# Optimization experiments

Hardware: AMD Instinct MI355X
Metric: run time of the kernel (lower is better)

## Reference

```python
import jax, jax.numpy as jnp
import numpy as np

SIG = 10
C = 0.0
STD = 1.0
N_ATOMS = 21
N_TRAIN = 8192
DESC = N_ATOMS * (N_ATOMS - 1) // 2  # 210
M = 64


def setup_inputs() -> dict:
    key = jax.random.key(0)
    k1, k2, k3 = jax.random.split(key, 3)
    Rs = jax.random.normal(k1, (M, N_ATOMS, 3), dtype=jnp.float32)
    xs_train = jax.random.uniform(k2, (N_TRAIN, DESC), dtype=jnp.float32)
    Jx_alphas = jax.random.normal(k3, (N_TRAIN, DESC), dtype=jnp.float32)
    return {"Rs": Rs, "xs_train": xs_train, "Jx_alphas": Jx_alphas}


def reference(Rs, xs_train, Jx_alphas):
    sig = SIG
    q = np.sqrt(5.0) / sig
    n = N_ATOMS
    # pairwise atom displacements / distances: [M, n, n, 3], [M, n, n]
    diffs = Rs[:, :, None, :] - Rs[:, None, :, :]
    dists = jnp.linalg.norm(diffs, axis=-1)
    eye = jnp.eye(n, dtype=bool)
    dists = jnp.where(eye, jnp.inf, dists)  # kill diagonal
    i, j = np.tril_indices(n, k=-1)
    xs = 1.0 / dists[:, i, j]                       # [M, D] inverse-distance descriptor
    x_diffs = q * xs[:, None, :] - q * xs_train     # [M, T, D]
    x_dists = jnp.linalg.norm(x_diffs, axis=-1)     # [M, T]
    exp_xs = (5.0 / (3.0 * sig ** 2)) * jnp.exp(-x_dists)
    dot = jnp.einsum('mtd,td->mt', x_diffs, Jx_alphas)
    exp_xs_1 = exp_xs * (1.0 + x_dists)
    F1s_x = jnp.einsum('mt,mtd->md', exp_xs * dot, x_diffs)  # [M, D]
    F2s_x = exp_xs_1 @ Jx_alphas                              # [M, D]
    Fs_x = (F1s_x - F2s_x) * STD
    # expand_tril: scatter D lower-tri values to symmetric [M, n, n], zero diag
    full = jnp.zeros((Fs_x.shape[0], n, n), dtype=Fs_x.dtype)
    full = full.at[:, i, j].set(Fs_x).at[:, j, i].set(Fs_x)
    Fs = jnp.einsum('mab,mabc->mac', full / dists ** 3, diffs)  # diag: 0/inf -> 0
    Es = jnp.sum(exp_xs_1 * dot, axis=-1) / q
    Es = C + Es * STD
    return Es, Fs
```

## Files before the change

kernel.cpp:

```cpp
#include <hip/hip_runtime.h>
#include <math.h>

#define NA   21
#define NM   64
#define ND   210
#define DP   224
#define NT   8192
#define NCH  28
#define KS2  32

#define QC 0.22360679774997896f
#define KE 0.016666666666666666f

typedef short bf8 __attribute__((ext_vector_type(8)));
typedef float f4  __attribute__((ext_vector_type(4)));

#define O_XF   0u
#define O_JF   917504u
#define O_XFT  1835008u
#define O_JFT  2752512u
#define O_W1   3670016u
#define O_E1   3932160u
#define O_AF   4194304u
#define O_QG   4201472u
#define O_NTT  4215808u
#define O_CJ   4224000u
#define O_NX   4232192u
#define O_PB   4261056u
#define O_ESP  5178560u
#define O_WAP  5211328u

__device__ __forceinline__ unsigned short f2bf(float f) {
    unsigned u = __float_as_uint(f);
    u += 0x7fffu + ((u >> 16) & 1u);
    return (unsigned short)(u >> 16);
}
__device__ __forceinline__ float bf2f(unsigned short h) {
    return __uint_as_float((unsigned)h << 16);
}

__device__ __forceinline__ void d_to_ij(int d, int& i, int& j) {
    int ii = (int)((1.0f + sqrtf(1.0f + 8.0f * (float)d)) * 0.5f);
    while (ii * (ii - 1) / 2 > d) --ii;
    while ((ii + 1) * ii / 2 <= d) ++ii;
    i = ii;
    j = d - ii * (ii - 1) / 2;
}

__global__ __launch_bounds__(256) void k_prep(
    const float* __restrict__ Rs, const float* __restrict__ xs,
    const float* __restrict__ Jx,
    unsigned short* __restrict__ Xf, unsigned short* __restrict__ Jf,
    unsigned short* __restrict__ XfT, unsigned short* __restrict__ JfT,
    unsigned short* __restrict__ Af, float* __restrict__ qxsG,
    float* __restrict__ nx, float* __restrict__ nt, float* __restrict__ cJ) {
    const int b = blockIdx.x, tid = threadIdx.x;
    __shared__ float lds[2 * 16 * 210];

    if (b < 512) {
        const int t0 = b * 16;
        const float4* sx = (const float4*)(xs + (size_t)t0 * ND);
        const float4* sj = (const float4*)(Jx + (size_t)t0 * ND);
#pragma unroll
        for (int k = 0; k < 4; ++k) {
            const int i = k * 256 + tid;
            if (i < 840) {
                ((float4*)lds)[i] = sx[i];
                ((float4*)(lds + 3360))[i] = sj[i];
            }
        }
        __syncthreads();
#pragma unroll
        for (int k = 0; k < 7; ++k) {
            const int idx = k * 256 + tid;
            if (idx < 896) {
                const int arr = idx / 448;
                const int rem = idx - arr * 448;
                const int kq = rem >> 4, colt = rem & 15;
                const float* src = lds + arr * 3360 + colt * 210;
                const float sc = arr ? 1.0f : QC;
                union { unsigned short us[8]; uint4 v; } u;
#pragma unroll
                for (int i = 0; i < 8; ++i) {
                    const int d = kq * 8 + i;
                    u.us[i] = (d < ND) ? f2bf(sc * src[d]) : (unsigned short)0;
                }
                *(uint4*)((arr ? Jf : Xf) + ((size_t)(b * NCH + kq) * 16 + colt) * 8) = u.v;
            } else {
                const int idx2 = idx - 896;
                const int arr = idx2 / 448;
                const int rem = idx2 - arr * 448;
                const int dtile = rem >> 5;
                const int rem2 = rem & 31;
                const int tql = rem2 >> 4, col = rem2 & 15;
                const int d = dtile * 16 + col;
                const float* src = lds + arr * 3360 + tql * 8 * 210;
                const float sc = arr ? 1.0f : QC;
                union { unsigned short us[8]; uint4 v; } u;
#pragma unroll
                for (int i = 0; i < 8; ++i)
                    u.us[i] = (d < ND) ? f2bf(sc * src[i * 210 + d])
                                       : (unsigned short)0;
                const size_t off = ((size_t)(dtile * 1024 + b * 2 + tql) * 16 + col) * 8;
                *(uint4*)((arr ? JfT : XfT) + off) = u.v;
            }
        }
        const int tt = tid >> 4, l = tid & 15;
        const float* xr = lds + tt * 210;
        const float* jr = lds + 3360 + tt * 210;
        float sn = 0.0f, sc2 = 0.0f;
        for (int c = l; c < ND; c += 16) {
            float x = bf2f(f2bf(QC * xr[c]));
            float j = bf2f(f2bf(jr[c]));
            sn = fmaf(x, x, sn);
            sc2 = fmaf(x, j, sc2);
        }
#pragma unroll
        for (int off = 1; off < 16; off <<= 1) {
            sn += __shfl_xor(sn, off);
            sc2 += __shfl_xor(sc2, off);
        }
        if (l == 0) {
            nt[t0 + tt] = sn;
            cJ[t0 + tt] = sc2;
        }
    } else {
        const int m = b - 512;
        float* R = lds;
        float* red = lds + 64;
        if (tid < NA * 3) R[tid] = Rs[m * NA * 3 + tid];
        __syncthreads();
        float local = 0.0f;
        if (tid < DP) {
            float vr = 0.0f;
            unsigned short hv = 0;
            if (tid < ND) {
                int i, j; d_to_ij(tid, i, j);
                float dx = R[i * 3] - R[j * 3];
                float dy = R[i * 3 + 1] - R[j * 3 + 1];
                float dz = R[i * 3 + 2] - R[j * 3 + 2];
                float v = QC / sqrtf(dx * dx + dy * dy + dz * dz);
                hv = f2bf(v);
                vr = bf2f(hv);
            }
            Af[(((m >> 4) * NCH + (tid >> 3)) * 16 + (m & 15)) * 8 + (tid & 7)] = hv;
            qxsG[(tid >> 2) * 256 + m * 4 + (tid & 3)] = vr;
            local = vr * vr;
        }
        red[tid] = local;
        __syncthreads();
        for (int s = 128; s > 0; s >>= 1) {
            if (tid < s) red[tid] += red[tid + s];
            __syncthreads();
        }
        if (tid == 0) nx[m] = red[0];
    }
}

__global__ __launch_bounds__(256) void k_stage1(
    const unsigned short* __restrict__ Af, const unsigned short* __restrict__ Xf,
    const unsigned short* __restrict__ Jf, const float* __restrict__ nt,
    const float* __restrict__ cJ, const float* __restrict__ nx,
    unsigned short* __restrict__ w1f, unsigned short* __restrict__ e1f,
    float* __restrict__ EsPart, float* __restrict__ WaPart) {
    const int tid = threadIdx.x;
    const int lane = tid & 63;
    const int w = tid >> 6;
    const int col = lane & 15, quad = lane >> 4;
    const int ttile = blockIdx.x;
    __shared__ float Dw[64][17];
    __shared__ float De[64][17];

    const unsigned short* ap = Af + ((size_t)(w * NCH + quad) * 16 + col) * 8;
    const unsigned short* xp = Xf + ((size_t)(ttile * NCH + quad) * 16 + col) * 8;
    const unsigned short* jp = Jf + ((size_t)(ttile * NCH + quad) * 16 + col) * 8;

    bf8 af[7];
#pragma unroll
    for (int kc = 0; kc < 7; ++kc) af[kc] = *(const bf8*)(ap + kc * 512);

    bf8 bx[2], bj[2];
    bx[0] = *(const bf8*)xp;
    bj[0] = *(const bf8*)jp;
    bx[1] = *(const bf8*)(xp + 512);
    bj[1] = *(const bf8*)(jp + 512);

    f4 c1 = {0.f, 0.f, 0.f, 0.f};
    f4 c2 = {0.f, 0.f, 0.f, 0.f};
#pragma unroll
    for (int kc = 0; kc < 7; ++kc) {
        const int s = kc & 1;
        c1 = __builtin_amdgcn_mfma_f32_16x16x32_bf16(af[kc], bx[s], c1, 0, 0, 0);
        c2 = __builtin_amdgcn_mfma_f32_16x16x32_bf16(af[kc], bj[s], c2, 0, 0, 0);
        if (kc < 5) {
            bx[s] = *(const bf8*)(xp + (kc + 2) * 512);
            bj[s] = *(const bf8*)(jp + (kc + 2) * 512);
        }
    }

    const int t = ttile * 16 + col;
    const float ntv = nt[t], cjv = cJ[t];
    float esA[4], wlA[4];
#pragma unroll
    for (int r = 0; r < 4; ++r) {
        const int m = w * 16 + quad * 4 + r;
        float sq = fmaxf(nx[m] - 2.0f * c1[r] + ntv, 0.0f);
        float xd = sqrtf(sq);
        float e = KE * expf(-xd);
        float dotv = c2[r] - cjv;
        float wv = e * dotv;
        float ev = e * (1.0f + xd);
        Dw[m][col] = wv;
        De[m][col] = ev;
        esA[r] = ev * dotv;
        wlA[r] = wv;
    }
    __syncthreads();
    {
        const int aidx = tid >> 7;
        const int c = tid & 127;
        const int mtile = c >> 5, tql = (c >> 4) & 1, colm = c & 15;
        const float* srcD = aidx ? &De[0][0] : &Dw[0][0];
        unsigned short* dst = aidx ? e1f : w1f;
        const int m = mtile * 16 + colm;
        union { unsigned short us[8]; uint4 v; } u;
#pragma unroll
        for (int i = 0; i < 8; ++i) u.us[i] = f2bf(srcD[m * 17 + tql * 8 + i]);
        const size_t off = ((size_t)(mtile * 1024 + ttile * 2 + tql) * 16 + colm) * 8;
        *(uint4*)(dst + off) = u.v;
    }
#pragma unroll
    for (int r = 0; r < 4; ++r) {
        float e = esA[r], wl = wlA[r];
#pragma unroll
        for (int off = 1; off < 16; off <<= 1) {
            e += __shfl_xor(e, off);
            wl += __shfl_xor(wl, off);
        }
        if (col == 0) {
            const int m = w * 16 + quad * 4 + r;
            EsPart[(size_t)m * 512 + ttile] = e;
            WaPart[(size_t)m * 512 + ttile] = wl;
        }
    }
}

__global__ __launch_bounds__(256) void k_stage2(
    const unsigned short* __restrict__ w1f, const unsigned short* __restrict__ e1f,
    const unsigned short* __restrict__ XfT, const unsigned short* __restrict__ JfT,
    float* __restrict__ Pbuf) {
    const int tid = threadIdx.x;
    const int lane = tid & 63;
    const int w = tid >> 6;
    const int col = lane & 15, quad = lane >> 4;
    const int dt = blockIdx.x;
    const int by = blockIdx.y;

    const unsigned short* awp = w1f + ((size_t)(w * 1024 + by * 32 + quad) * 16 + col) * 8;
    const unsigned short* aep = e1f + ((size_t)(w * 1024 + by * 32 + quad) * 16 + col) * 8;
    const unsigned short* bxp = XfT + ((size_t)(dt * 1024 + by * 32 + quad) * 16 + col) * 8;
    const unsigned short* bjp = JfT + ((size_t)(dt * 1024 + by * 32 + quad) * 16 + col) * 8;

    bf8 aw[2], ae[2], bx[2], bj[2];
    aw[0] = *(const bf8*)awp;         ae[0] = *(const bf8*)aep;
    bx[0] = *(const bf8*)bxp;         bj[0] = *(const bf8*)bjp;
    aw[1] = *(const bf8*)(awp + 512); ae[1] = *(const bf8*)(aep + 512);
    bx[1] = *(const bf8*)(bxp + 512); bj[1] = *(const bf8*)(bjp + 512);

    f4 dA = {0.f, 0.f, 0.f, 0.f};
    f4 dB = {0.f, 0.f, 0.f, 0.f};
#pragma unroll
    for (int kk = 0; kk < 8; ++kk) {
        const int s = kk & 1;
        dA = __builtin_amdgcn_mfma_f32_16x16x32_bf16(aw[s], bx[s], dA, 0, 0, 0);
        dB = __builtin_amdgcn_mfma_f32_16x16x32_bf16(ae[s], bj[s], dB, 0, 0, 0);
        if (kk < 6) {
            aw[s] = *(const bf8*)(awp + (kk + 2) * 512);
            ae[s] = *(const bf8*)(aep + (kk + 2) * 512);
            bx[s] = *(const bf8*)(bxp + (kk + 2) * 512);
            bj[s] = *(const bf8*)(bjp + (kk + 2) * 512);
        }
    }
    float* p = Pbuf + (size_t)by * 28672 + dt * 16 + col;
#pragma unroll
    for (int r = 0; r < 4; ++r) {
        const int m = w * 16 + quad * 4 + r;
        p[m * DP] = dA[r];
        p[14336 + m * DP] = dB[r];
    }
}

__global__ void k_final(const float* __restrict__ Rs, const float* __restrict__ qxsG,
                        const float* __restrict__ Pbuf, const float* __restrict__ EsPart,
                        const float* __restrict__ WaPart, float* __restrict__ out) {
    int m = blockIdx.x, tid = threadIdx.x;
    __shared__ float R[NA * 3];
    __shared__ float Ff[NA][NA];
    __shared__ float redE[256];
    __shared__ float redW[256];
    __shared__ float ABs[DP];
    if (tid < NA * 3) R[tid] = Rs[m * NA * 3 + tid];
    if (tid < NA) Ff[tid][tid] = 0.0f;
    if (tid < DP) {
        const float* p0 = Pbuf + (size_t)m * DP + tid;
        float s1 = 0.0f, s2 = 0.0f;
#pragma unroll
        for (int ks = 0; ks < KS2; ++ks) {
            s1 += p0[(size_t)ks * 28672];
            s2 += p0[(size_t)ks * 28672 + 14336];
        }
        ABs[tid] = s1 + s2;
    }
    {
        const float2 ep = ((const float2*)(EsPart + (size_t)m * 512))[tid];
        const float2 wp = ((const float2*)(WaPart + (size_t)m * 512))[tid];
        redE[tid] = ep.x + ep.y;
        redW[tid] = wp.x + wp.y;
    }
    __syncthreads();
    for (int s = 128; s > 0; s >>= 1) {
        if (tid < s) {
            redE[tid] += redE[tid + s];
            redW[tid] += redW[tid + s];
        }
        __syncthreads();
    }
    const float Wa = redW[0];
    if (tid < ND) {
        int i, j; d_to_ij(tid, i, j);
        float dx = R[i * 3] - R[j * 3];
        float dy = R[i * 3 + 1] - R[j * 3 + 1];
        float dz = R[i * 3 + 2] - R[j * 3 + 2];
        float dist2 = dx * dx + dy * dy + dz * dz;
        float fsx = qxsG[(tid >> 2) * 256 + m * 4 + (tid & 3)] * Wa - ABs[tid];
        float f = fsx / (dist2 * sqrtf(dist2));
        Ff[i][j] = f;
        Ff[j][i] = f;
    }
    __syncthreads();
    if (tid < NA * 3) {
        int a = tid / 3, c = tid % 3;
        float s = 0.0f;
        for (int b = 0; b < NA; ++b) {
            if (b == a) continue;
            s += Ff[a][b] * (R[a * 3 + c] - R[b * 3 + c]);
        }
        out[NM + m * NA * 3 + tid] = s;
    }
    if (tid == 0) out[m] = redE[0] / QC;
}

extern "C" void kernel_launch(void* const* d_in, const int* in_sizes, int n_in,
                              void* d_out, int out_size, void* d_ws, size_t ws_size,
                              hipStream_t stream) {
    const float* Rs = (const float*)d_in[0];
    const float* xs_train = (const float*)d_in[1];
    const float* Jx_alphas = (const float*)d_in[2];
    float* out = (float*)d_out;
    float* ws = (float*)d_ws;

    unsigned short* Xf  = (unsigned short*)(ws + O_XF);
    unsigned short* Jf  = (unsigned short*)(ws + O_JF);
    unsigned short* XfT = (unsigned short*)(ws + O_XFT);
    unsigned short* JfT = (unsigned short*)(ws + O_JFT);
    unsigned short* w1f = (unsigned short*)(ws + O_W1);
    unsigned short* e1f = (unsigned short*)(ws + O_E1);
    unsigned short* Af  = (unsigned short*)(ws + O_AF);
    float* qxsG   = ws + O_QG;
    float* nt     = ws + O_NTT;
    float* cJ     = ws + O_CJ;
    float* nx     = ws + O_NX;
    float* Pbuf   = ws + O_PB;
    float* EsPart = ws + O_ESP;
    float* WaPart = ws + O_WAP;

    k_prep<<<576, 256, 0, stream>>>(Rs, xs_train, Jx_alphas, Xf, Jf, XfT, JfT,
                                    Af, qxsG, nx, nt, cJ);
    k_stage1<<<512, 256, 0, stream>>>(Af, Xf, Jf, nt, cJ, nx, w1f, e1f, EsPart, WaPart);
    k_stage2<<<dim3(14, KS2), 256, 0, stream>>>(w1f, e1f, XfT, JfT, Pbuf);
    k_final<<<NM, 256, 0, stream>>>(Rs, qxsG, Pbuf, EsPart, WaPart, out);
}
```

Baseline: 92.78 us.

## Fuse train-data bf16 conversion into stage1 via swizzled LDS tiles

Splits the geometry part of the prep kernel into its own small kernel and moves the xs/Jx conversion into the stage1 kernel. Each stage1 block now loads its 16 training rows, converts them to bf16 in an XOR-swizzled LDS buffer, computes the norms locally, and feeds the MFMA B operands from LDS. This drops the Xf/Jf/nt/cJ global round trip. The cost is more LDS per block and extra in-kernel conversion work ahead of the MFMA loop.

```diff
diff --git a/kernel.cpp b/kernel.cpp
--- a/kernel.cpp
+++ b/kernel.cpp
@@ -15,16 +15,12 @@
 typedef short bf8 __attribute__((ext_vector_type(8)));
 typedef float f4  __attribute__((ext_vector_type(4)));
 
-#define O_XF   0u
-#define O_JF   917504u
 #define O_XFT  1835008u
 #define O_JFT  2752512u
 #define O_W1   3670016u
 #define O_E1   3932160u
 #define O_AF   4194304u
 #define O_QG   4201472u
-#define O_NTT  4215808u
-#define O_CJ   4224000u
 #define O_NX   4232192u
 #define O_PB   4261056u
 #define O_ESP  5178560u
@@ -47,144 +43,139 @@
     j = d - ii * (ii - 1) / 2;
 }
 
-__global__ __launch_bounds__(256) void k_prep(
-    const float* __restrict__ Rs, const float* __restrict__ xs,
-    const float* __restrict__ Jx,
-    unsigned short* __restrict__ Xf, unsigned short* __restrict__ Jf,
+__global__ __launch_bounds__(256) void k_geom(
+    const float* __restrict__ Rs, unsigned short* __restrict__ Af,
+    float* __restrict__ qxsG, float* __restrict__ nx) {
+    const int m = blockIdx.x, tid = threadIdx.x;
+    __shared__ float R[NA * 3];
+    __shared__ float red[256];
+    if (tid < NA * 3) R[tid] = Rs[m * NA * 3 + tid];
+    __syncthreads();
+    float local = 0.0f;
+    if (tid < DP) {
+        float vr = 0.0f;
+        unsigned short hv = 0;
+        if (tid < ND) {
+            int i, j; d_to_ij(tid, i, j);
+            float dx = R[i * 3] - R[j * 3];
+            float dy = R[i * 3 + 1] - R[j * 3 + 1];
+            float dz = R[i * 3 + 2] - R[j * 3 + 2];
+            float v = QC / sqrtf(dx * dx + dy * dy + dz * dz);
+            hv = f2bf(v);
+            vr = bf2f(hv);
+        }
+        Af[(((m >> 4) * NCH + (tid >> 3)) * 16 + (m & 15)) * 8 + (tid & 7)] = hv;
+        qxsG[(tid >> 2) * 256 + m * 4 + (tid & 3)] = vr;
+        local = vr * vr;
+    }
+    red[tid] = local;
+    __syncthreads();
+    for (int s = 128; s > 0; s >>= 1) {
+        if (tid < s) red[tid] += red[tid + s];
+        __syncthreads();
+    }
+    if (tid == 0) nx[m] = red[0];
+}
+
+__global__ __launch_bounds__(256) void k_s1p(
+    const float* __restrict__ xs, const float* __restrict__ Jx,
+    const unsigned short* __restrict__ Af, const float* __restrict__ nxg,
     unsigned short* __restrict__ XfT, unsigned short* __restrict__ JfT,
-    unsigned short* __restrict__ Af, float* __restrict__ qxsG,
-    float* __restrict__ nx, float* __restrict__ nt, float* __restrict__ cJ) {
-    const int b = blockIdx.x, tid = threadIdx.x;
-    __shared__ float lds[2 * 16 * 210];
-
-    if (b < 512) {
-        const int t0 = b * 16;
-        const float4* sx = (const float4*)(xs + (size_t)t0 * ND);
-        const float4* sj = (const float4*)(Jx + (size_t)t0 * ND);
-#pragma unroll
-        for (int k = 0; k < 4; ++k) {
-            const int i = k * 256 + tid;
-            if (i < 840) {
-                ((float4*)lds)[i] = sx[i];
-                ((float4*)(lds + 3360))[i] = sj[i];
-            }
-        }
-        __syncthreads();
-#pragma unroll
-        for (int k = 0; k < 7; ++k) {
-            const int idx = k * 256 + tid;
-            if (idx < 896) {
-                const int arr = idx / 448;
-                const int rem = idx - arr * 448;
-                const int kq = rem >> 4, colt = rem & 15;
-                const float* src = lds + arr * 3360 + colt * 210;
-                const float sc = arr ? 1.0f : QC;
-                union { unsigned short us[8]; uint4 v; } u;
-#pragma unroll
-                for (int i = 0; i < 8; ++i) {
-                    const int d = kq * 8 + i;
-                    u.us[i] = (d < ND) ? f2bf(sc * src[d]) : (unsigned short)0;
-                }
-                *(uint4*)((arr ? Jf : Xf) + ((size_t)(b * NCH + kq) * 16 + colt) * 8) = u.v;
-            } else {
-                const int idx2 = idx - 896;
-                const int arr = idx2 / 448;
-                const int rem = idx2 - arr * 448;
-                const int dtile = rem >> 5;
-                const int rem2 = rem & 31;
-                const int tql = rem2 >> 4, col = rem2 & 15;
-                const int d = dtile * 16 + col;
-                const float* src = lds + arr * 3360 + tql * 8 * 210;
-                const float sc = arr ? 1.0f : QC;
-                union { unsigned short us[8]; uint4 v; } u;
-#pragma unroll
-                for (int i = 0; i < 8; ++i)
-                    u.us[i] = (d < ND) ? f2bf(sc * src[i * 210 + d])
-                                       : (unsigned short)0;
-                const size_t off = ((size_t)(dtile * 1024 + b * 2 + tql) * 16 + col) * 8;
-                *(uint4*)((arr ? JfT : XfT) + off) = u.v;
-            }
-        }
-        const int tt = tid >> 4, l = tid & 15;
-        const float* xr = lds + tt * 210;
-        const float* jr = lds + 3360 + tt * 210;
-        float sn = 0.0f, sc2 = 0.0f;
-        for (int c = l; c < ND; c += 16) {
-            float x = bf2f(f2bf(QC * xr[c]));
-            float j = bf2f(f2bf(jr[c]));
-            sn = fmaf(x, x, sn);
-            sc2 = fmaf(x, j, sc2);
-        }
-#pragma unroll
-        for (int off = 1; off < 16; off <<= 1) {
-            sn += __shfl_xor(sn, off);
-            sc2 += __shfl_xor(sc2, off);
-        }
-        if (l == 0) {
-            nt[t0 + tt] = sn;
-            cJ[t0 + tt] = sc2;
-        }
-    } else {
-        const int m = b - 512;
-        float* R = lds;
-        float* red = lds + 64;
-        if (tid < NA * 3) R[tid] = Rs[m * NA * 3 + tid];
-        __syncthreads();
-        float local = 0.0f;
-        if (tid < DP) {
-            float vr = 0.0f;
-            unsigned short hv = 0;
-            if (tid < ND) {
-                int i, j; d_to_ij(tid, i, j);
-                float dx = R[i * 3] - R[j * 3];
-                float dy = R[i * 3 + 1] - R[j * 3 + 1];
-                float dz = R[i * 3 + 2] - R[j * 3 + 2];
-                float v = QC / sqrtf(dx * dx + dy * dy + dz * dz);
-                hv = f2bf(v);
-                vr = bf2f(hv);
-            }
-            Af[(((m >> 4) * NCH + (tid >> 3)) * 16 + (m & 15)) * 8 + (tid & 7)] = hv;
-            qxsG[(tid >> 2) * 256 + m * 4 + (tid & 3)] = vr;
-            local = vr * vr;
-        }
-        red[tid] = local;
-        __syncthreads();
-        for (int s = 128; s > 0; s >>= 1) {
-            if (tid < s) red[tid] += red[tid + s];
-            __syncthreads();
-        }
-        if (tid == 0) nx[m] = red[0];
-    }
-}
-
-__global__ __launch_bounds__(256) void k_stage1(
-    const unsigned short* __restrict__ Af, const unsigned short* __restrict__ Xf,
-    const unsigned short* __restrict__ Jf, const float* __restrict__ nt,
-    const float* __restrict__ cJ, const float* __restrict__ nx,
     unsigned short* __restrict__ w1f, unsigned short* __restrict__ e1f,
     float* __restrict__ EsPart, float* __restrict__ WaPart) {
-    const int tid = threadIdx.x;
+    const int b = blockIdx.x, tid = threadIdx.x;
     const int lane = tid & 63;
     const int w = tid >> 6;
     const int col = lane & 15, quad = lane >> 4;
-    const int ttile = blockIdx.x;
+
+    __shared__ unsigned short xJh[2 * 16 * DP];
     __shared__ float Dw[64][17];
     __shared__ float De[64][17];
+    __shared__ float ntL[16], cjL[16];
+    char* xB = (char*)xJh;
 
     const unsigned short* ap = Af + ((size_t)(w * NCH + quad) * 16 + col) * 8;
-    const unsigned short* xp = Xf + ((size_t)(ttile * NCH + quad) * 16 + col) * 8;
-    const unsigned short* jp = Jf + ((size_t)(ttile * NCH + quad) * 16 + col) * 8;
-
     bf8 af[7];
 #pragma unroll
     for (int kc = 0; kc < 7; ++kc) af[kc] = *(const bf8*)(ap + kc * 512);
-
+    float nxv[4];
+#pragma unroll
+    for (int r = 0; r < 4; ++r) nxv[r] = nxg[w * 16 + quad * 4 + r];
+
+    if (tid < 224) {
+        const int arr = tid / 112, rem = tid - arr * 112;
+        const int t = rem / 7, k2 = rem - t * 7;
+        *(unsigned*)(xB + arr * 7168 +
+                     (((unsigned)(t * 448 + 420 + k2 * 4)) ^ ((unsigned)((t & 7) << 4)))) = 0u;
+    }
+    const float2* sx = (const float2*)(xs + (size_t)b * 16 * ND);
+    const float2* sj = (const float2*)(Jx + (size_t)b * 16 * ND);
+#pragma unroll
+    for (int k = 0; k < 7; ++k) {
+        const int p = k * 256 + tid;
+        if (p < 1680) {
+            const float2 vx = sx[p];
+            const float2 vj = sj[p];
+            const int t = p / 105;
+            const unsigned bo = ((unsigned)(4 * p + 28 * t)) ^ ((unsigned)((t & 7) << 4));
+            *(unsigned*)(xB + bo) =
+                (unsigned)f2bf(QC * vx.x) | ((unsigned)f2bf(QC * vx.y) << 16);
+            *(unsigned*)(xB + 7168 + bo) =
+                (unsigned)f2bf(vj.x) | ((unsigned)f2bf(vj.y) << 16);
+        }
+    }
+    __syncthreads();
+
+    {
+        const int tt = tid >> 4, l = tid & 15;
+        const unsigned swt = (unsigned)((tt & 7) << 4);
+        float sn = 0.0f, sc2 = 0.0f;
+#pragma unroll
+        for (int c = l; c < DP; c += 16) {
+            const unsigned off = ((unsigned)(tt * 448 + 2 * c)) ^ swt;
+            const float x = bf2f(*(const unsigned short*)(xB + off));
+            const float jv = bf2f(*(const unsigned short*)(xB + 7168 + off));
+            sn = fmaf(x, x, sn);
+            sc2 = fmaf(x, jv, sc2);
+        }
+#pragma unroll
+        for (int o = 1; o < 16; o <<= 1) {
+            sn += __shfl_xor(sn, o);
+            sc2 += __shfl_xor(sc2, o);
+        }
+        if (l == 0) { ntL[tt] = sn; cjL[tt] = sc2; }
+    }
+#pragma unroll
+    for (int k = 0; k < 4; ++k) {
+        const int idx = k * 256 + tid;
+        if (idx < 896) {
+            const int arr = idx / 448;
+            const int rem = idx - arr * 448;
+            const int dtile = rem >> 5;
+            const int rem2 = rem & 31;
+            const int tql = rem2 >> 4, cc = rem2 & 15;
+            const int dbyte = 2 * (dtile * 16 + cc);
+            union { unsigned short us[8]; uint4 v; } u;
+#pragma unroll
+            for (int i = 0; i < 8; ++i) {
+                const int t = tql * 8 + i;
+                const unsigned off =
+                    ((unsigned)(t * 448 + dbyte)) ^ ((unsigned)((t & 7) << 4));
+                u.us[i] = *(const unsigned short*)(xB + arr * 7168 + off);
+            }
+            const size_t o2 = ((size_t)(dtile * 1024 + b * 2 + tql) * 16 + cc) * 8;
+            *(uint4*)((arr ? JfT : XfT) + o2) = u.v;
+        }
+    }
+    __syncthreads();
+
+    const unsigned base0 = (unsigned)(col * 448 + quad * 16);
+    const unsigned swc = (unsigned)((col & 7) << 4);
     bf8 bx[2], bj[2];
-    bx[0] = *(const bf8*)xp;
-    bj[0] = *(const bf8*)jp;
-    bx[1] = *(const bf8*)(xp + 512);
-    bj[1] = *(const bf8*)(jp + 512);
-
+    bx[0] = *(const bf8*)(xB + (base0 ^ swc));
+    bj[0] = *(const bf8*)(xB + 7168 + (base0 ^ swc));
+    bx[1] = *(const bf8*)(xB + ((base0 + 64) ^ swc));
+    bj[1] = *(const bf8*)(xB + 7168 + ((base0 + 64) ^ swc));
     f4 c1 = {0.f, 0.f, 0.f, 0.f};
     f4 c2 = {0.f, 0.f, 0.f, 0.f};
 #pragma unroll
@@ -193,18 +184,17 @@
         c1 = __builtin_amdgcn_mfma_f32_16x16x32_bf16(af[kc], bx[s], c1, 0, 0, 0);
         c2 = __builtin_amdgcn_mfma_f32_16x16x32_bf16(af[kc], bj[s], c2, 0, 0, 0);
         if (kc < 5) {
-            bx[s] = *(const bf8*)(xp + (kc + 2) * 512);
-            bj[s] = *(const bf8*)(jp + (kc + 2) * 512);
-        }
-    }
-
-    const int t = ttile * 16 + col;
-    const float ntv = nt[t], cjv = cJ[t];
+            bx[s] = *(const bf8*)(xB + ((base0 + (kc + 2) * 64) ^ swc));
+            bj[s] = *(const bf8*)(xB + 7168 + ((base0 + (kc + 2) * 64) ^ swc));
+        }
+    }
+
+    const float ntv = ntL[col], cjv = cjL[col];
     float esA[4], wlA[4];
 #pragma unroll
     for (int r = 0; r < 4; ++r) {
         const int m = w * 16 + quad * 4 + r;
-        float sq = fmaxf(nx[m] - 2.0f * c1[r] + ntv, 0.0f);
+        float sq = fmaxf(nxv[r] - 2.0f * c1[r] + ntv, 0.0f);
         float xd = sqrtf(sq);
         float e = KE * expf(-xd);
         float dotv = c2[r] - cjv;
@@ -226,21 +216,21 @@
         union { unsigned short us[8]; uint4 v; } u;
 #pragma unroll
         for (int i = 0; i < 8; ++i) u.us[i] = f2bf(srcD[m * 17 + tql * 8 + i]);
-        const size_t off = ((size_t)(mtile * 1024 + ttile * 2 + tql) * 16 + colm) * 8;
+        const size_t off = ((size_t)(mtile * 1024 + b * 2 + tql) * 16 + colm) * 8;
         *(uint4*)(dst + off) = u.v;
     }
 #pragma unroll
     for (int r = 0; r < 4; ++r) {
         float e = esA[r], wl = wlA[r];
 #pragma unroll
-        for (int off = 1; off < 16; off <<= 1) {
-            e += __shfl_xor(e, off);
-            wl += __shfl_xor(wl, off);
+        for (int o = 1; o < 16; o <<= 1) {
+            e += __shfl_xor(e, o);
+            wl += __shfl_xor(wl, o);
         }
         if (col == 0) {
             const int m = w * 16 + quad * 4 + r;
-            EsPart[(size_t)m * 512 + ttile] = e;
-            WaPart[(size_t)m * 512 + ttile] = wl;
+            EsPart[(size_t)m * 512 + b] = e;
+            WaPart[(size_t)m * 512 + b] = wl;
         }
     }
 }
@@ -359,24 +349,20 @@
     float* out = (float*)d_out;
     float* ws = (float*)d_ws;
 
-    unsigned short* Xf  = (unsigned short*)(ws + O_XF);
-    unsigned short* Jf  = (unsigned short*)(ws + O_JF);
     unsigned short* XfT = (unsigned short*)(ws + O_XFT);
     unsigned short* JfT = (unsigned short*)(ws + O_JFT);
     unsigned short* w1f = (unsigned short*)(ws + O_W1);
     unsigned short* e1f = (unsigned short*)(ws + O_E1);
     unsigned short* Af  = (unsigned short*)(ws + O_AF);
     float* qxsG   = ws + O_QG;
-    float* nt     = ws + O_NTT;
-    float* cJ     = ws + O_CJ;
     float* nx     = ws + O_NX;
     float* Pbuf   = ws + O_PB;
     float* EsPart = ws + O_ESP;
     float* WaPart = ws + O_WAP;
 
-    k_prep<<<576, 256, 0, stream>>>(Rs, xs_train, Jx_alphas, Xf, Jf, XfT, JfT,
-                                    Af, qxsG, nx, nt, cJ);
-    k_stage1<<<512, 256, 0, stream>>>(Af, Xf, Jf, nt, cJ, nx, w1f, e1f, EsPart, WaPart);
+    k_geom<<<NM, 256, 0, stream>>>(Rs, Af, qxsG, nx);
+    k_s1p<<<512, 256, 0, stream>>>(xs_train, Jx_alphas, Af, nx, XfT, JfT,
+                                   w1f, e1f, EsPart, WaPart);
     k_stage2<<<dim3(14, KS2), 256, 0, stream>>>(w1f, e1f, XfT, JfT, Pbuf);
     k_final<<<NM, 256, 0, stream>>>(Rs, qxsG, Pbuf, EsPart, WaPart, out);
 }
```

Result: faster. 90.25 us (-2.7%).
